# Kernel tuning notes

Hardware: AMD Instinct MI355X
Metric: run time of the kernel (lower is better)

Reference implementation:

```python
import jax, jax.numpy as jnp
import numpy as np

DT = 0.1  # fixed dt offset from init_kwargs


def setup_inputs() -> dict:
    key = jax.random.key(0)
    ks = jax.random.split(key, 8)
    B_, L, D, N = 4, 4096, 128, 16
    s = 1.0 / np.sqrt(D)
    # S4D-Real init: A_n = -(n+1), repeated over input_dim (random_init=False)
    A = jnp.broadcast_to(-(jnp.arange(N, dtype=jnp.float32) + 1.0), (D, N))
    return {
        "x": jax.random.normal(ks[0], (B_, L, D), dtype=jnp.float32),
        "A": A,
        "Wb": jax.random.uniform(ks[1], (N, D), minval=-s, maxval=s, dtype=jnp.float32),
        "bb": jax.random.uniform(ks[2], (N,), minval=-s, maxval=s, dtype=jnp.float32),
        "Wc": jax.random.uniform(ks[3], (N, D), minval=-s, maxval=s, dtype=jnp.float32),
        "bc": jax.random.uniform(ks[4], (N,), minval=-s, maxval=s, dtype=jnp.float32),
        "Wd": jax.random.uniform(ks[5], (1, D), minval=-s, maxval=s, dtype=jnp.float32),
        "bd": jax.random.uniform(ks[6], (1,), minval=-s, maxval=s, dtype=jnp.float32),
    }


def reference(x, A, Wb, bb, Wc, bc, Wd, bd):
    # x: [B, L, D]; A: [D, N]
    Bp = x @ Wb.T + bb                                   # [B, L, N]  (self.sb)
    C = x @ Wc.T + bc                                    # [B, L, N]  (self.sc)
    # DeltaNetwork: softplus(Linear(x)) + dt, repeated over input_dim
    delta = jax.nn.softplus(x @ Wd.T + bd) + DT          # [B, L, 1]
    delta = jnp.broadcast_to(delta, x.shape)             # [B, L, D]
    # discretize: A_bar = exp(dt*A); B_bar = (1 - exp(-dt*A)) * (dt x B)
    dA = delta[..., None] * A                            # [B, L, D, N]
    A_bar = jnp.exp(dA)
    Bx = (1.0 - jnp.exp(-dA)) * delta[..., None] * Bp[:, :, None, :] * x[..., None]  # B_bar * x_t

    def step(h, inp):
        A_t, Bx_t, C_t = inp                             # [B,D,N],[B,D,N],[B,N]
        h = A_t * h + Bx_t
        y_t = jnp.sum(h * C_t[:, None, :], axis=-1)      # [B, D]
        return h, y_t

    h0 = jnp.zeros((x.shape[0], x.shape[2], A.shape[1]), x.dtype)
    _, y = jax.lax.scan(
        step, h0,
        (A_bar.transpose(1, 0, 2, 3), Bx.transpose(1, 0, 2, 3), C.transpose(1, 0, 2)),
    )
    return y.transpose(1, 0, 2)                          # [B, L, D]
```

## Files before the change

kernel.cpp:

```cpp
#include <hip/hip_runtime.h>
#include <math.h>

#define B_ 4
#define L_ 4096
#define D_ 128
#define N_ 16
#define DT_ 0.1f
#define CHUNK_ 32
#define NC_ 128

#define ABAR_OFF 0
#define COEF_OFF (ABAR_OFF + 262144)
#define CC_OFF   (COEF_OFF + 262144)
#define HL_OFF   (CC_OFF + 262144)
#define H0_OFF   (HL_OFF + 1048576)
#define P_OFF    (H0_OFF + 1048576)

__global__ __launch_bounds__(256) void k1_proj(const float* __restrict__ x,
                                               const float* __restrict__ A,
                                               const float* __restrict__ Wb,
                                               const float* __restrict__ bb,
                                               const float* __restrict__ Wc,
                                               const float* __restrict__ bc,
                                               const float* __restrict__ Wd,
                                               const float* __restrict__ bd,
                                               float* __restrict__ ws) {
    __shared__ float xs[64][129];
    __shared__ float proj[64][18];

    float* abar_o = ws + ABAR_OFF;
    float* coef_o = ws + COEF_OFF;
    float* cc_o   = ws + CC_OFF;

    const int t = threadIdx.x;
    const int bt = blockIdx.x & 1;
    const size_t row0 = (size_t)(blockIdx.x >> 1) * 64;

    const float4* xg = (const float4*)(x + row0 * 128);
    for (int i = t; i < 2048; i += 256) {
        float4 v = xg[i];
        int r = i >> 5;
        int c0 = (i & 31) << 2;
        xs[r][c0]     = v.x;
        xs[r][c0 + 1] = v.y;
        xs[r][c0 + 2] = v.z;
        xs[r][c0 + 3] = v.w;
    }
    __syncthreads();

    const int w = __builtin_amdgcn_readfirstlane(t >> 6);
    const int lane = t & 63;

    const float* cbase = (bt == 0 ? Wb : Wc) + (size_t)w * 4 * 128;
    float a0 = 0.f, a1 = 0.f, a2 = 0.f, a3 = 0.f;
#pragma unroll 8
    for (int k = 0; k < 128; ++k) {
        float xv = xs[lane][k];
        a0 = fmaf(xv, cbase[k],       a0);
        a1 = fmaf(xv, cbase[128 + k], a1);
        a2 = fmaf(xv, cbase[256 + k], a2);
        a3 = fmaf(xv, cbase[384 + k], a3);
    }
    proj[lane][w * 4]     = a0;
    proj[lane][w * 4 + 1] = a1;
    proj[lane][w * 4 + 2] = a2;
    proj[lane][w * 4 + 3] = a3;
    if (bt == 0 && w == 3) {
        float ad = 0.f;
#pragma unroll 8
        for (int k = 0; k < 128; ++k) ad = fmaf(xs[lane][k], Wd[k], ad);
        proj[lane][16] = ad;
    }
    __syncthreads();

    const int r = t & 63;
    const int g = t >> 6;
    const int n0 = g * 4;
    const size_t orow = (row0 + (size_t)r) * 16 + n0;

    if (bt == 0) {
        float zd = proj[r][16] + bd[0];
        float sp = fmaxf(zd, 0.f) + log1pf(expf(-fabsf(zd)));
        float delta = sp + DT_;
        float4 ab4, cf4;
        { float Bp = proj[r][n0]     + bb[n0];     float dA = delta * A[n0];
          ab4.x = expf(dA); cf4.x = (1.f - expf(-dA)) * delta * Bp; }
        { float Bp = proj[r][n0 + 1] + bb[n0 + 1]; float dA = delta * A[n0 + 1];
          ab4.y = expf(dA); cf4.y = (1.f - expf(-dA)) * delta * Bp; }
        { float Bp = proj[r][n0 + 2] + bb[n0 + 2]; float dA = delta * A[n0 + 2];
          ab4.z = expf(dA); cf4.z = (1.f - expf(-dA)) * delta * Bp; }
        { float Bp = proj[r][n0 + 3] + bb[n0 + 3]; float dA = delta * A[n0 + 3];
          ab4.w = expf(dA); cf4.w = (1.f - expf(-dA)) * delta * Bp; }
        *(float4*)(abar_o + orow) = ab4;
        *(float4*)(coef_o + orow) = cf4;
    } else {
        float4 cv4;
        cv4.x = proj[r][n0]     + bc[n0];
        cv4.y = proj[r][n0 + 1] + bc[n0 + 1];
        cv4.z = proj[r][n0 + 2] + bc[n0 + 2];
        cv4.w = proj[r][n0 + 3] + bc[n0 + 3];
        *(float4*)(cc_o + orow) = cv4;
    }
}

__global__ __launch_bounds__(256, 4) void k2a_chunk(const float* __restrict__ x,
                                                    float* __restrict__ ws) {
    const float* abar = ws + ABAR_OFF;
    const float* coef = ws + COEF_OFF;
    float* hL = ws + HL_OFF;
    float* Pp = ws + P_OFF;

    const int gw = blockIdx.x * 4 + (threadIdx.x >> 6);
    const int lane = threadIdx.x & 63;
    const int b = gw >> 10;
    const int dgrp = (gw >> 7) & 7;
    const int c = gw & 127;
    const int ng = lane >> 4;
    const int dq = lane & 15;
    const int d = dgrp * 16 + dq;
    const int l0 = c * CHUNK_;
    const float* pa = abar + ((size_t)b * L_ + l0) * 16 + ng * 4;
    const float* pc = coef + ((size_t)b * L_ + l0) * 16 + ng * 4;
    const float* px = x + ((size_t)b * L_ + l0) * 128 + d;

    float h0v = 0.f, h1v = 0.f, h2v = 0.f, h3v = 0.f;
    float P0 = 1.f, P1 = 1.f, P2 = 1.f, P3 = 1.f;

    float4 a4 = *(const float4*)pa;
    float4 c4 = *(const float4*)pc;
    float xv = px[0];
#pragma unroll 8
    for (int t = 0; t < CHUNK_ - 1; ++t) {
        float4 an = *(const float4*)(pa + (t + 1) * 16);
        float4 cn = *(const float4*)(pc + (t + 1) * 16);
        float xn = px[(t + 1) * 128];
        h0v = fmaf(a4.x, h0v, c4.x * xv);
        h1v = fmaf(a4.y, h1v, c4.y * xv);
        h2v = fmaf(a4.z, h2v, c4.z * xv);
        h3v = fmaf(a4.w, h3v, c4.w * xv);
        P0 *= a4.x; P1 *= a4.y; P2 *= a4.z; P3 *= a4.w;
        a4 = an; c4 = cn; xv = xn;
    }
    h0v = fmaf(a4.x, h0v, c4.x * xv);
    h1v = fmaf(a4.y, h1v, c4.y * xv);
    h2v = fmaf(a4.z, h2v, c4.z * xv);
    h3v = fmaf(a4.w, h3v, c4.w * xv);
    P0 *= a4.x; P1 *= a4.y; P2 *= a4.z; P3 *= a4.w;

    *(float4*)(hL + (((size_t)(b * NC_ + c)) * 128 + d) * 16 + ng * 4) =
        make_float4(h0v, h1v, h2v, h3v);
    if (dq == 0) {
        *(float4*)(Pp + ((size_t)(b * NC_ + c)) * 16 + ng * 4) =
            make_float4(P0, P1, P2, P3);
    }
}

__global__ __launch_bounds__(256, 4) void k2b_combine(float* __restrict__ ws) {
    const float* hL = ws + HL_OFF;
    const float* Pp = ws + P_OFF;
    float* h0 = ws + H0_OFF;
    const int tid = blockIdx.x * 256 + threadIdx.x;
    const int b = tid >> 11;
    const int dn = tid & 2047;
    const int n = tid & 15;

    const float* hp = hL + (size_t)b * NC_ * 2048 + dn;
    const float* pp = Pp + (size_t)b * NC_ * 16 + n;
    float* op = h0 + (size_t)b * NC_ * 2048 + dn;

    float h = 0.f;
    op[0] = 0.f;
#pragma unroll 8
    for (int c = 0; c < NC_ - 1; ++c) {
        float hl = hp[(size_t)c * 2048];
        float p  = pp[(size_t)c * 16];
        h = fmaf(p, h, hl);
        op[(size_t)(c + 1) * 2048] = h;
    }
}

__global__ __launch_bounds__(256, 4) void k2c_scan(const float* __restrict__ x,
                                                   const float* __restrict__ ws,
                                                   float* __restrict__ y) {
    const float* abar = ws + ABAR_OFF;
    const float* coef = ws + COEF_OFF;
    const float* cc   = ws + CC_OFF;
    const float* h0   = ws + H0_OFF;

    const int gw = blockIdx.x * 4 + (threadIdx.x >> 6);
    const int lane = threadIdx.x & 63;
    const int b = gw >> 10;
    const int dgrp = (gw >> 7) & 7;
    const int c = gw & 127;
    const int ng = lane >> 4;
    const int dq = lane & 15;
    const int d = dgrp * 16 + dq;
    const int l0 = c * CHUNK_;
    const float* pa = abar + ((size_t)b * L_ + l0) * 16 + ng * 4;
    const float* pc = coef + ((size_t)b * L_ + l0) * 16 + ng * 4;
    const float* pC = cc   + ((size_t)b * L_ + l0) * 16 + ng * 4;
    const float* px = x + ((size_t)b * L_ + l0) * 128 + d;
    float* py = y + ((size_t)b * L_ + l0) * 128 + d;

    float4 h4 = *(const float4*)(h0 + (((size_t)(b * NC_ + c)) * 128 + d) * 16 + ng * 4);
    float h0v = h4.x, h1v = h4.y, h2v = h4.z, h3v = h4.w;

    float4 a4 = *(const float4*)pa;
    float4 c4 = *(const float4*)pc;
    float4 C4 = *(const float4*)pC;
    float xv = px[0];
#pragma unroll 8
    for (int t = 0; t < CHUNK_; ++t) {
        float4 an, cn, Cn;
        float xn;
        if (t < CHUNK_ - 1) {
            an = *(const float4*)(pa + (t + 1) * 16);
            cn = *(const float4*)(pc + (t + 1) * 16);
            Cn = *(const float4*)(pC + (t + 1) * 16);
            xn = px[(t + 1) * 128];
        }
        h0v = fmaf(a4.x, h0v, c4.x * xv);
        h1v = fmaf(a4.y, h1v, c4.y * xv);
        h2v = fmaf(a4.z, h2v, c4.z * xv);
        h3v = fmaf(a4.w, h3v, c4.w * xv);
        float yv = h0v * C4.x + h1v * C4.y + h2v * C4.z + h3v * C4.w;
        yv += __shfl_xor(yv, 16);
        yv += __shfl_xor(yv, 32);
        if (ng == 0) py[t * 128] = yv;
        if (t < CHUNK_ - 1) { a4 = an; c4 = cn; C4 = Cn; xv = xn; }
    }
}

extern "C" void kernel_launch(void* const* d_in, const int* in_sizes, int n_in,
                              void* d_out, int out_size, void* d_ws, size_t ws_size,
                              hipStream_t stream) {
    const float* x  = (const float*)d_in[0];
    const float* A  = (const float*)d_in[1];
    const float* Wb = (const float*)d_in[2];
    const float* bb = (const float*)d_in[3];
    const float* Wc = (const float*)d_in[4];
    const float* bc = (const float*)d_in[5];
    const float* Wd = (const float*)d_in[6];
    const float* bd = (const float*)d_in[7];
    float* ws = (float*)d_ws;
    float* y  = (float*)d_out;

    k1_proj<<<512, 256, 0, stream>>>(x, A, Wb, bb, Wc, bc, Wd, bd, ws);
    k2a_chunk<<<1024, 256, 0, stream>>>(x, ws);
    k2b_combine<<<32, 256, 0, stream>>>(ws);
    k2c_scan<<<1024, 256, 0, stream>>>(x, ws, y);
}
```

Before: 145.7 us.

## Compute local-chunk outputs in first pass and correct with carry-in update

The first chunk pass now also produces the zero-initial-state outputs and per-timestep weights C·cumprod(Abar). After the chunk combine, a light update kernel adds the carried-in state contribution (W·h0) to each output instead of rerunning the full recurrence. This removes the second sequential scan over the chunk and its re-reads of abar, coef and x. In exchange it writes and reads an extra partial-output buffer the size of y, plus the weight buffer.

```diff
diff --git a/kernel.cpp b/kernel.cpp
--- a/kernel.cpp
+++ b/kernel.cpp
@@ -10,11 +10,13 @@
 #define NC_ 128
 
 #define ABAR_OFF 0
-#define COEF_OFF (ABAR_OFF + 262144)
-#define CC_OFF   (COEF_OFF + 262144)
-#define HL_OFF   (CC_OFF + 262144)
-#define H0_OFF   (HL_OFF + 1048576)
-#define P_OFF    (H0_OFF + 1048576)
+#define COEF_OFF 262144
+#define CC_OFF   524288
+#define HL_OFF   786432
+#define H0_OFF   1835008
+#define P_OFF    2883584
+#define W_OFF    2891776
+#define YP_OFF   3153920
 
 __global__ __launch_bounds__(256) void k1_proj(const float* __restrict__ x,
                                                const float* __restrict__ A,
@@ -107,85 +109,11 @@
                                                     float* __restrict__ ws) {
     const float* abar = ws + ABAR_OFF;
     const float* coef = ws + COEF_OFF;
+    const float* cc   = ws + CC_OFF;
     float* hL = ws + HL_OFF;
     float* Pp = ws + P_OFF;
-
-    const int gw = blockIdx.x * 4 + (threadIdx.x >> 6);
-    const int lane = threadIdx.x & 63;
-    const int b = gw >> 10;
-    const int dgrp = (gw >> 7) & 7;
-    const int c = gw & 127;
-    const int ng = lane >> 4;
-    const int dq = lane & 15;
-    const int d = dgrp * 16 + dq;
-    const int l0 = c * CHUNK_;
-    const float* pa = abar + ((size_t)b * L_ + l0) * 16 + ng * 4;
-    const float* pc = coef + ((size_t)b * L_ + l0) * 16 + ng * 4;
-    const float* px = x + ((size_t)b * L_ + l0) * 128 + d;
-
-    float h0v = 0.f, h1v = 0.f, h2v = 0.f, h3v = 0.f;
-    float P0 = 1.f, P1 = 1.f, P2 = 1.f, P3 = 1.f;
-
-    float4 a4 = *(const float4*)pa;
-    float4 c4 = *(const float4*)pc;
-    float xv = px[0];
-#pragma unroll 8
-    for (int t = 0; t < CHUNK_ - 1; ++t) {
-        float4 an = *(const float4*)(pa + (t + 1) * 16);
-        float4 cn = *(const float4*)(pc + (t + 1) * 16);
-        float xn = px[(t + 1) * 128];
-        h0v = fmaf(a4.x, h0v, c4.x * xv);
-        h1v = fmaf(a4.y, h1v, c4.y * xv);
-        h2v = fmaf(a4.z, h2v, c4.z * xv);
-        h3v = fmaf(a4.w, h3v, c4.w * xv);
-        P0 *= a4.x; P1 *= a4.y; P2 *= a4.z; P3 *= a4.w;
-        a4 = an; c4 = cn; xv = xn;
-    }
-    h0v = fmaf(a4.x, h0v, c4.x * xv);
-    h1v = fmaf(a4.y, h1v, c4.y * xv);
-    h2v = fmaf(a4.z, h2v, c4.z * xv);
-    h3v = fmaf(a4.w, h3v, c4.w * xv);
-    P0 *= a4.x; P1 *= a4.y; P2 *= a4.z; P3 *= a4.w;
-
-    *(float4*)(hL + (((size_t)(b * NC_ + c)) * 128 + d) * 16 + ng * 4) =
-        make_float4(h0v, h1v, h2v, h3v);
-    if (dq == 0) {
-        *(float4*)(Pp + ((size_t)(b * NC_ + c)) * 16 + ng * 4) =
-            make_float4(P0, P1, P2, P3);
-    }
-}
-
-__global__ __launch_bounds__(256, 4) void k2b_combine(float* __restrict__ ws) {
-    const float* hL = ws + HL_OFF;
-    const float* Pp = ws + P_OFF;
-    float* h0 = ws + H0_OFF;
-    const int tid = blockIdx.x * 256 + threadIdx.x;
-    const int b = tid >> 11;
-    const int dn = tid & 2047;
-    const int n = tid & 15;
-
-    const float* hp = hL + (size_t)b * NC_ * 2048 + dn;
-    const float* pp = Pp + (size_t)b * NC_ * 16 + n;
-    float* op = h0 + (size_t)b * NC_ * 2048 + dn;
-
-    float h = 0.f;
-    op[0] = 0.f;
-#pragma unroll 8
-    for (int c = 0; c < NC_ - 1; ++c) {
-        float hl = hp[(size_t)c * 2048];
-        float p  = pp[(size_t)c * 16];
-        h = fmaf(p, h, hl);
-        op[(size_t)(c + 1) * 2048] = h;
-    }
-}
-
-__global__ __launch_bounds__(256, 4) void k2c_scan(const float* __restrict__ x,
-                                                   const float* __restrict__ ws,
-                                                   float* __restrict__ y) {
-    const float* abar = ws + ABAR_OFF;
-    const float* coef = ws + COEF_OFF;
-    const float* cc   = ws + CC_OFF;
-    const float* h0   = ws + H0_OFF;
+    float* wo = ws + W_OFF;
+    float* yp = ws + YP_OFF;
 
     const int gw = blockIdx.x * 4 + (threadIdx.x >> 6);
     const int lane = threadIdx.x & 63;
@@ -200,10 +128,12 @@
     const float* pc = coef + ((size_t)b * L_ + l0) * 16 + ng * 4;
     const float* pC = cc   + ((size_t)b * L_ + l0) * 16 + ng * 4;
     const float* px = x + ((size_t)b * L_ + l0) * 128 + d;
-    float* py = y + ((size_t)b * L_ + l0) * 128 + d;
-
-    float4 h4 = *(const float4*)(h0 + (((size_t)(b * NC_ + c)) * 128 + d) * 16 + ng * 4);
-    float h0v = h4.x, h1v = h4.y, h2v = h4.z, h3v = h4.w;
+    float* pw = wo + ((size_t)b * L_ + l0) * 16 + ng * 4;
+    float* py = yp + ((size_t)b * L_ + l0) * 128 + d;
+
+    float h0v = 0.f, h1v = 0.f, h2v = 0.f, h3v = 0.f;
+    float P0 = 1.f, P1 = 1.f, P2 = 1.f, P3 = 1.f;
+    const bool wlane = (dgrp == 0) && (dq == 0);
 
     float4 a4 = *(const float4*)pa;
     float4 c4 = *(const float4*)pc;
@@ -219,15 +149,111 @@
             Cn = *(const float4*)(pC + (t + 1) * 16);
             xn = px[(t + 1) * 128];
         }
+        P0 *= a4.x; P1 *= a4.y; P2 *= a4.z; P3 *= a4.w;
         h0v = fmaf(a4.x, h0v, c4.x * xv);
         h1v = fmaf(a4.y, h1v, c4.y * xv);
         h2v = fmaf(a4.z, h2v, c4.z * xv);
         h3v = fmaf(a4.w, h3v, c4.w * xv);
+        if (wlane) {
+            *(float4*)(pw + t * 16) = make_float4(C4.x * P0, C4.y * P1,
+                                                  C4.z * P2, C4.w * P3);
+        }
         float yv = h0v * C4.x + h1v * C4.y + h2v * C4.z + h3v * C4.w;
         yv += __shfl_xor(yv, 16);
         yv += __shfl_xor(yv, 32);
         if (ng == 0) py[t * 128] = yv;
         if (t < CHUNK_ - 1) { a4 = an; c4 = cn; C4 = Cn; xv = xn; }
+    }
+
+    *(float4*)(hL + (((size_t)(b * NC_ + c)) * 128 + d) * 16 + ng * 4) =
+        make_float4(h0v, h1v, h2v, h3v);
+    if (dq == 0) {
+        *(float4*)(Pp + ((size_t)(b * NC_ + c)) * 16 + ng * 4) =
+            make_float4(P0, P1, P2, P3);
+    }
+}
+
+__global__ __launch_bounds__(256, 4) void k2b_combine(float* __restrict__ ws) {
+    const float* hL = ws + HL_OFF;
+    const float* Pp = ws + P_OFF;
+    float* h0 = ws + H0_OFF;
+    const int tid = blockIdx.x * 256 + threadIdx.x;
+    const int b = tid >> 11;
+    const int dn = tid & 2047;
+    const int n = tid & 15;
+
+    const float* hp = hL + (size_t)b * NC_ * 2048 + dn;
+    const float* pp = Pp + (size_t)b * NC_ * 16 + n;
+    float* op = h0 + (size_t)b * NC_ * 2048 + dn;
+
+    float h = 0.f;
+    op[0] = 0.f;
+#pragma unroll 8
+    for (int c = 0; c < NC_ - 1; ++c) {
+        float hl = hp[(size_t)c * 2048];
+        float p  = pp[(size_t)c * 16];
+        h = fmaf(p, h, hl);
+        op[(size_t)(c + 1) * 2048] = h;
+    }
+}
+
+__global__ __launch_bounds__(256, 4) void k2c_update(const float* __restrict__ ws,
+                                                     float* __restrict__ y) {
+    __shared__ float h0s[128][17];
+    __shared__ float wcs[32][17];
+
+    const int blk = blockIdx.x;
+    const int b = blk >> 7;
+    const int c = blk & 127;
+    const int t = threadIdx.x;
+
+    const float4* h0g = (const float4*)(ws + H0_OFF + (size_t)blk * 2048);
+    for (int i = t; i < 512; i += 256) {
+        float4 v = h0g[i];
+        int d = i >> 2, n0 = (i & 3) << 2;
+        h0s[d][n0] = v.x; h0s[d][n0 + 1] = v.y;
+        h0s[d][n0 + 2] = v.z; h0s[d][n0 + 3] = v.w;
+    }
+    const float4* wg = (const float4*)(ws + W_OFF + ((size_t)b * L_ + c * CHUNK_) * 16);
+    for (int i = t; i < 128; i += 256) {
+        float4 v = wg[i];
+        int tt = i >> 2, n0 = (i & 3) << 2;
+        wcs[tt][n0] = v.x; wcs[tt][n0 + 1] = v.y;
+        wcs[tt][n0 + 2] = v.z; wcs[tt][n0 + 3] = v.w;
+    }
+    __syncthreads();
+
+    const int tt = t >> 3;
+    const int dblk = (t & 7) << 4;
+
+    const float w0 = wcs[tt][0],  w1 = wcs[tt][1],  w2 = wcs[tt][2],  w3 = wcs[tt][3];
+    const float w4 = wcs[tt][4],  w5 = wcs[tt][5],  w6 = wcs[tt][6],  w7 = wcs[tt][7];
+    const float w8 = wcs[tt][8],  w9 = wcs[tt][9],  wA = wcs[tt][10], wB = wcs[tt][11];
+    const float wC = wcs[tt][12], wD = wcs[tt][13], wE = wcs[tt][14], wF = wcs[tt][15];
+
+    const size_t rowoff = ((size_t)b * L_ + c * CHUNK_ + tt) * 128 + dblk;
+    const float4* yp4 = (const float4*)(ws + YP_OFF + rowoff);
+    float4* yo4 = (float4*)(y + rowoff);
+
+#pragma unroll
+    for (int q = 0; q < 4; ++q) {
+        float4 acc = yp4[q];
+        float* ap = (float*)&acc;
+#pragma unroll
+        for (int j = 0; j < 4; ++j) {
+            const float* hr = h0s[dblk + q * 4 + j];
+            float s = ap[j];
+            s = fmaf(w0, hr[0],  s); s = fmaf(w1, hr[1],  s);
+            s = fmaf(w2, hr[2],  s); s = fmaf(w3, hr[3],  s);
+            s = fmaf(w4, hr[4],  s); s = fmaf(w5, hr[5],  s);
+            s = fmaf(w6, hr[6],  s); s = fmaf(w7, hr[7],  s);
+            s = fmaf(w8, hr[8],  s); s = fmaf(w9, hr[9],  s);
+            s = fmaf(wA, hr[10], s); s = fmaf(wB, hr[11], s);
+            s = fmaf(wC, hr[12], s); s = fmaf(wD, hr[13], s);
+            s = fmaf(wE, hr[14], s); s = fmaf(wF, hr[15], s);
+            ap[j] = s;
+        }
+        yo4[q] = acc;
     }
 }
 
@@ -248,5 +274,5 @@
     k1_proj<<<512, 256, 0, stream>>>(x, A, Wb, bb, Wc, bc, Wd, bd, ws);
     k2a_chunk<<<1024, 256, 0, stream>>>(x, ws);
     k2b_combine<<<32, 256, 0, stream>>>(ws);
-    k2c_scan<<<1024, 256, 0, stream>>>(x, ws, y);
-}
+    k2c_update<<<512, 256, 0, stream>>>(ws, y);
+}
```

New measurement: 147.7 us. No clear change (+1.3%).
